# Performance work log

Hardware: AMD Instinct MI355X
Metric: run time of the kernel (lower is better)

## Reference

```python
import jax, jax.numpy as jnp
import numpy as np

GENRES = 20; TAGS = 1000; GTAGS = 1128; MOVIES = 20000; YEARS = 120; TBINS = 128
B = 1024; HIST = 50; PH = 256; OD = 128
EG = 8; ET = 16; EGT = 16; EM = 32; EY = 8; EUG = 32; ETS = 4
PAD = MOVIES  # padding index; context buffers have MOVIES+1 rows, last row = zeros


def setup_inputs():
    ks = iter(jax.random.split(jax.random.key(0), 64))
    nrm = lambda shp, s=0.1: (s * jax.random.normal(next(ks), shp)).astype(jnp.float32)
    P = MOVIES + 1
    genome_ctx = jax.random.uniform(next(ks), (P, GTAGS), dtype=jnp.float32).at[-1].set(0.0)
    genre_ctx = jax.random.uniform(next(ks), (P, GENRES), dtype=jnp.float32).at[-1].set(0.0)
    tag_ctx = jax.random.uniform(next(ks), (P, TAGS), dtype=jnp.float32).at[-1].set(0.0)
    year_ctx = jax.random.randint(next(ks), (P,), 0, YEARS).at[-1].set(0)
    return dict(
        user_genre_contexts=jax.random.uniform(next(ks), (B, GENRES), dtype=jnp.float32),
        user_watch_history=jax.random.randint(next(ks), (B, HIST), 0, P),
        user_watch_history_ratings=5.0 * jax.random.uniform(next(ks), (B, HIST), dtype=jnp.float32),
        timestamps=jax.random.randint(next(ks), (B,), 0, TBINS),
        target_movieId=jax.random.randint(next(ks), (B,), 0, MOVIES),
        genome_ctx=genome_ctx, genre_ctx=genre_ctx, tag_ctx=tag_ctx, year_ctx=year_ctx,
        item_emb=nrm((P, EM), 0.01).at[-1].set(0.0),  # padding_idx row zeroed
        year_emb_tab=nrm((YEARS, EY), 0.01),
        ts_emb_tab=nrm((TBINS, ETS), 0.01),
        w_item=nrm((EM, EM)), b_item=jnp.zeros((EM,), jnp.float32),
        w_genre=nrm((GENRES, EG)), b_genre=jnp.zeros((EG,), jnp.float32),
        w_tag=nrm((TAGS, ET)), b_tag=jnp.zeros((ET,), jnp.float32),
        w_genome=nrm((GTAGS, EGT)), b_genome=jnp.zeros((EGT,), jnp.float32),
        w_year=nrm((EY, EY)), b_year=jnp.zeros((EY,), jnp.float32),
        w_ugenre=nrm((GENRES, EUG)), b_ugenre=jnp.zeros((EUG,), jnp.float32),
        w_ts=nrm((ETS, ETS)), b_ts=jnp.zeros((ETS,), jnp.float32),
        w_up1=nrm((OD + EGT + EUG + ETS, PH)), b_up1=jnp.zeros((PH,), jnp.float32),
        w_up2=nrm((PH, OD)), b_up2=jnp.zeros((OD,), jnp.float32),
        w_ip1=nrm((EG + ET + EGT + EM + EY, PH)), b_ip1=jnp.zeros((PH,), jnp.float32),
        w_ip2=nrm((PH, OD)), b_ip2=jnp.zeros((OD,), jnp.float32),
    )


def reference(user_genre_contexts, user_watch_history, user_watch_history_ratings,
              timestamps, target_movieId, genome_ctx, genre_ctx, tag_ctx, year_ctx,
              item_emb, year_emb_tab, ts_emb_tab,
              w_item, b_item, w_genre, b_genre, w_tag, b_tag, w_genome, b_genome,
              w_year, b_year, w_ugenre, b_ugenre, w_ts, b_ts,
              w_up1, b_up1, w_up2, b_up2, w_ip1, b_ip1, w_ip2, b_ip2):
    lt = lambda x, W, b: jnp.tanh(x @ W + b)

    def item_tower(mg, mt, mgt, yr, ids):
        # concat of five small Linear+Tanh towers, then 2-layer projection MLP
        cat = jnp.concatenate([
            lt(mg, w_genre, b_genre), lt(mt, w_tag, b_tag), lt(mgt, w_genome, b_genome),
            lt(item_emb[ids], w_item, b_item), lt(year_emb_tab[yr], w_year, b_year)], axis=-1)
        return jax.nn.relu(cat @ w_ip1 + b_ip1) @ w_ip2 + b_ip2

    Bn, Hn = user_watch_history.shape
    pad_mask = (user_watch_history != PAD).astype(jnp.float32)[..., None]       # (B,H,1)
    rating_weights = user_watch_history_ratings[..., None] * pad_mask            # (B,H,1)
    weight_sum = jnp.clip(jnp.abs(rating_weights).sum(axis=1), 1e-6)             # (B,1)

    # item pool: full item-tower embeddings of watched movies, rating-weighted avg
    flat = user_watch_history.reshape(-1)
    embs = item_tower(genre_ctx[flat], tag_ctx[flat], genome_ctx[flat],
                      year_ctx[flat], flat).reshape(Bn, Hn, OD)
    item_pool = (embs * rating_weights).sum(axis=1) / weight_sum                 # (B,OD)

    # genome pool (kept separately in use_item_pool_for_history mode)
    genome_embs = lt(genome_ctx[user_watch_history], w_genome, b_genome)         # (B,H,EGT)
    genome_emb = (genome_embs * rating_weights).sum(axis=1) / weight_sum

    genre_emb = lt(user_genre_contexts, w_ugenre, b_ugenre)
    ts_emb = lt(ts_emb_tab[timestamps], w_ts, b_ts)
    user_cat = jnp.concatenate([item_pool, genome_emb, genre_emb, ts_emb], axis=1)
    user = jax.nn.relu(user_cat @ w_up1 + b_up1) @ w_up2 + b_up2                 # (B,OD)

    item = item_tower(genre_ctx[target_movieId], tag_ctx[target_movieId],
                      genome_ctx[target_movieId], year_ctx[target_movieId], target_movieId)
    return jnp.einsum('bd,bd->b', user, item)
```

## Files before the change

### kernel.cpp

```cpp
#include <hip/hip_runtime.h>
#include <hip/hip_bf16.h>

typedef __bf16 bf16x8 __attribute__((ext_vector_type(8)));
typedef __bf16 bf16x4 __attribute__((ext_vector_type(4)));
typedef float  f32x4  __attribute__((ext_vector_type(4)));

namespace {
constexpr int P       = 20001;
constexpr int NT_TILE = 1251;
constexpr int PROWS   = NT_TILE * 16;
constexpr int NGENRES = 20;
constexpr int NTAGS   = 1000;
constexpr int NGTAGS  = 1128;
constexpr int NB      = 1024;
constexpr int NH      = 50;
constexpr int PHID    = 256;
constexpr int OD      = 128;
constexpr int EG = 8, ET = 16, EGT = 16, EM = 32, EY = 8, EUG = 32, ETS = 4;
constexpr int PAD  = 20000;
constexpr int SC   = 104;
constexpr int SH   = 264;
constexpr int UC   = 192;
constexpr int UCS  = 200;
constexpr int KC_TAG  = 32;
constexpr int KC_GENF = 40;
constexpr int KC_IP1 = 3,  NT_IP1 = 16;
constexpr int KC_IP2 = 8,  NT_IP2 = 8;
constexpr int KC_UP1 = 6,  NT_UP1 = 16;
constexpr int KC_UP2 = 8,  NT_UP2 = 8;
}

static __device__ __forceinline__ f32x4 mfma16(bf16x8 a, bf16x8 b, f32x4 c) {
  return __builtin_amdgcn_mfma_f32_16x16x32_bf16(a, b, c, 0, 0, 0);
}

static __device__ __forceinline__ bf16x8 cvt8(float4 v0, float4 v1) {
  return (bf16x8){(__bf16)v0.x, (__bf16)v0.y, (__bf16)v0.z, (__bf16)v0.w,
                  (__bf16)v1.x, (__bf16)v1.y, (__bf16)v1.z, (__bf16)v1.w};
}

static __device__ __forceinline__ void gldlds(const void* g, void* l) {
  __builtin_amdgcn_global_load_lds(
      (const __attribute__((address_space(1))) void*)g,
      (__attribute__((address_space(3))) void*)l, 16, 0, 0);
}

__global__ __launch_bounds__(512) void setup_wf_kernel(
    const float* __restrict__ w_tag, const float* __restrict__ w_genome,
    const float* __restrict__ w_ip1, const float* __restrict__ w_ip2,
    const float* __restrict__ w_up1, const float* __restrict__ w_up2,
    __bf16* __restrict__ Wtf, __bf16* __restrict__ Wgf,
    __bf16* __restrict__ Wip1f, __bf16* __restrict__ Wip2f,
    __bf16* __restrict__ Wup1f, __bf16* __restrict__ Wup2f)
{
  const int b = blockIdx.x, t = threadIdx.x;
  const int l = t >> 3, j = t & 7;
  const int krow = (l >> 4) * 8 + j, l15 = l & 15;
  const float* src; __bf16* dst; int K, N, kc, nt;
  if (b < 32)        { src = w_tag;    dst = Wtf   + (long)b * 512;       K = NTAGS;  N = 16;  kc = b;      nt = 0; }
  else if (b < 72)   { int i = b - 32;  src = w_genome; dst = Wgf   + (long)i * 512; K = NGTAGS; N = 16;  kc = i;      nt = 0; }
  else if (b < 120)  { int i = b - 72;  src = w_ip1;    dst = Wip1f + (long)i * 512; K = 80;     N = 256; kc = i / 16; nt = i % 16; }
  else if (b < 184)  { int i = b - 120; src = w_ip2;    dst = Wip2f + (long)i * 512; K = 256;    N = 128; kc = i / 8;  nt = i % 8; }
  else if (b < 280)  { int i = b - 184; src = w_up1;    dst = Wup1f + (long)i * 512; K = 180;    N = 256; kc = i / 16; nt = i % 16; }
  else               { int i = b - 280; src = w_up2;    dst = Wup2f + (long)i * 512; K = 256;    N = 128; kc = i / 8;  nt = i % 8; }
  const int k = kc * 32 + krow, n = nt * 16 + l15;
  float v = (k < K) ? src[(long)k * N + n] : 0.f;
  dst[t] = (__bf16)v;
}

__global__ __launch_bounds__(256, 2) void tower_kernel(
    const float* __restrict__ tag_ctx, const float* __restrict__ genome_ctx,
    const float* __restrict__ genre_ctx, const int* __restrict__ year_ctx,
    const float* __restrict__ item_emb, const float* __restrict__ year_tab,
    const float* __restrict__ w_genre, const float* __restrict__ b_genre,
    const float* __restrict__ b_tag,   const float* __restrict__ b_genome,
    const float* __restrict__ w_item,  const float* __restrict__ b_item,
    const float* __restrict__ w_year,  const float* __restrict__ b_year,
    const float* __restrict__ b_ip1,   const float* __restrict__ b_ip2,
    const __bf16* __restrict__ Wtf,   const __bf16* __restrict__ Wgf,
    const __bf16* __restrict__ Wip1f, const __bf16* __restrict__ Wip2f,
    float* __restrict__ T, float* __restrict__ GT)
{
  __shared__ __align__(16) union {
    char tag[16 * 128 * 16];
    char gen[16 * 192 * 16];
  } u;
  __shared__ __align__(16) __bf16 s_cat[16][SC];
  __shared__ __align__(16) __bf16 s_h[16][SH];
  __shared__ __align__(16) f32x4  s_redT[3][64];
  __shared__ __align__(16) f32x4  s_redG[3][64];

  const int t = threadIdx.x, tile = blockIdx.x;
  const int wave = t >> 6, lane = t & 63, l15 = lane & 15, quad = lane >> 4;
  const int r = t >> 4, c16 = t & 15;
  const long rid_r = min(tile * 16 + r, P - 1);
  const int x = l15 & 7;

  f32x4 accT = {0.f, 0.f, 0.f, 0.f};
  f32x4 accG = {0.f, 0.f, 0.f, 0.f};

  #pragma unroll
  for (int h = 0; h < 2; ++h) {
    #pragma unroll
    for (int cc = 0; cc < 8; ++cc) {
      const int c = wave * 8 + cc, rr = c >> 1, i = c & 1;
      const long rid = min(tile * 16 + rr, P - 1);
      const char* rp = (const char*)tag_ctx + rid * (NTAGS * 4);
      const int gs = min(((i * 64 + lane) ^ (rr & 7)) + h * 128, 249);
      gldlds(rp + (long)gs * 16, u.tag + ((rr * 128 + i * 64) * 16));
    }
    asm volatile("s_waitcnt vmcnt(0)" ::: "memory");
    __syncthreads();
    #pragma unroll
    for (int c = 0; c < 4; ++c) {
      const int kcg = h * 16 + wave * 4 + c;
      const int j = (wave * 4 + c) * 8 + quad * 2;
      const float4* rowp = (const float4*)u.tag + l15 * 128;
      const float4 a0 = rowp[j ^ x];
      const float4 a1 = rowp[(j + 1) ^ x];
      bf16x8 tb = *(const bf16x8*)(Wtf + ((long)kcg * 64 + lane) * 8);
      accT = mfma16(cvt8(a0, a1), tb, accT);
    }
    __syncthreads();
  }

  #pragma unroll
  for (int h = 0; h < 2; ++h) {
    #pragma unroll
    for (int cc = 0; cc < 12; ++cc) {
      const int c = wave * 12 + cc, rr = c / 3, i = c % 3;
      const long rid = min(tile * 16 + rr, P - 1);
      const char* rp = (const char*)genome_ctx + rid * (NGTAGS * 4);
      const int gs = min(((i * 64 + lane) ^ (rr & 7)) + h * 160, 281);
      gldlds(rp + (long)gs * 16, u.gen + ((rr * 192 + i * 64) * 16));
    }
    asm volatile("s_waitcnt vmcnt(0)" ::: "memory");
    __syncthreads();
    #pragma unroll
    for (int c = 0; c < 5; ++c) {
      const int kcg = h * 20 + wave * 5 + c;
      const int j = (wave * 5 + c) * 8 + quad * 2;
      const float4* rowp = (const float4*)u.gen + l15 * 192;
      const float4 a0 = rowp[j ^ x];
      const float4 a1 = rowp[(j + 1) ^ x];
      bf16x8 gb = *(const bf16x8*)(Wgf + ((long)kcg * 64 + lane) * 8);
      accG = mfma16(cvt8(a0, a1), gb, accG);
    }
    __syncthreads();
  }

  if (wave > 0)  s_redT[wave - 1][lane] = accT;
  if (wave != 1) s_redG[wave ? wave - 1 : 0][lane] = accG;

  {
    const int m = r, j = c16;
    const long id = rid_r;
    if (j < 8) {
      const float* rg = genre_ctx + id * NGENRES;
      float a = b_genre[j];
      #pragma unroll
      for (int k = 0; k < NGENRES; ++k) a = fmaf(rg[k], w_genre[k * EG + j], a);
      s_cat[m][j] = (__bf16)tanhf(a);
      s_cat[m][80 + j] = (__bf16)0.f;
      s_cat[m][88 + j] = (__bf16)0.f;
    } else {
      const int jj = j - 8;
      const int yr = year_ctx[id];
      float a = b_year[jj];
      #pragma unroll
      for (int k = 0; k < EY; ++k)
        a = fmaf(year_tab[yr * EY + k], w_year[k * EY + jj], a);
      s_cat[m][72 + jj] = (__bf16)tanhf(a);
    }
    const float* e = item_emb + id * EM;
    float a0 = b_item[2 * j], a1 = b_item[2 * j + 1];
    #pragma unroll 8
    for (int k = 0; k < EM; ++k) {
      float ev = e[k];
      a0 = fmaf(ev, w_item[k * EM + 2 * j], a0);
      a1 = fmaf(ev, w_item[k * EM + 2 * j + 1], a1);
    }
    s_cat[m][40 + 2 * j]     = (__bf16)tanhf(a0);
    s_cat[m][40 + 2 * j + 1] = (__bf16)tanhf(a1);
  }
  __syncthreads();

  if (wave == 0) {
    accT += s_redT[0][lane]; accT += s_redT[1][lane]; accT += s_redT[2][lane];
    const float bt = b_tag[l15];
    #pragma unroll
    for (int r2 = 0; r2 < 4; ++r2)
      s_cat[quad * 4 + r2][EG + l15] = (__bf16)tanhf(accT[r2] + bt);
  } else if (wave == 1) {
    accG += s_redG[0][lane]; accG += s_redG[1][lane]; accG += s_redG[2][lane];
    const float bg = b_genome[l15];
    #pragma unroll
    for (int r2 = 0; r2 < 4; ++r2) {
      int m = quad * 4 + r2;
      float v = tanhf(accG[r2] + bg);
      s_cat[m][EG + ET + l15] = (__bf16)v;
      GT[(long)(tile * 16 + m) * EGT + l15] = v;
    }
  }
  __syncthreads();

  {
    bf16x8 af[KC_IP1];
    #pragma unroll
    for (int kc = 0; kc < KC_IP1; ++kc)
      af[kc] = *(const bf16x8*)&s_cat[l15][kc * 32 + quad * 8];
    #pragma unroll
    for (int nt = 0; nt < 4; ++nt) {
      const int n = wave * 64 + nt * 16 + l15;
      const float bb = b_ip1[n];
      f32x4 acc = {bb, bb, bb, bb};
      bf16x8 bfr[KC_IP1];
      #pragma unroll
      for (int kc = 0; kc < KC_IP1; ++kc)
        bfr[kc] = *(const bf16x8*)(Wip1f + ((long)(kc * NT_IP1 + wave * 4 + nt) * 64 + lane) * 8);
      #pragma unroll
      for (int kc = 0; kc < KC_IP1; ++kc)
        acc = mfma16(af[kc], bfr[kc], acc);
      #pragma unroll
      for (int r2 = 0; r2 < 4; ++r2)
        s_h[quad * 4 + r2][n] = (__bf16)fmaxf(acc[r2], 0.f);
    }
  }
  __syncthreads();

  {
    bf16x8 af[KC_IP2];
    #pragma unroll
    for (int kc = 0; kc < KC_IP2; ++kc)
      af[kc] = *(const bf16x8*)&s_h[l15][kc * 32 + quad * 8];
    #pragma unroll
    for (int nt = 0; nt < 2; ++nt) {
      const int n = wave * 32 + nt * 16 + l15;
      const float bb = b_ip2[n];
      f32x4 acc = {bb, bb, bb, bb};
      bf16x8 bfr[KC_IP2];
      #pragma unroll
      for (int kc = 0; kc < KC_IP2; ++kc)
        bfr[kc] = *(const bf16x8*)(Wip2f + ((long)(kc * NT_IP2 + wave * 2 + nt) * 64 + lane) * 8);
      #pragma unroll
      for (int kc = 0; kc < KC_IP2; ++kc)
        acc = mfma16(af[kc], bfr[kc], acc);
      #pragma unroll
      for (int r2 = 0; r2 < 4; ++r2)
        T[(long)(tile * 16 + quad * 4 + r2) * OD + n] = acc[r2];
    }
  }
}

__global__ __launch_bounds__(256) void user_pool_kernel(
    const float* __restrict__ ugc, const int* __restrict__ hist,
    const float* __restrict__ ratings, const int* __restrict__ tstamps,
    const float* __restrict__ ts_tab,
    const float* __restrict__ w_ugenre, const float* __restrict__ b_ugenre,
    const float* __restrict__ w_ts, const float* __restrict__ b_ts,
    const float* __restrict__ T, const float* __restrict__ GT,
    __bf16* __restrict__ Ucat)
{
  __shared__ float s_w[64];
  __shared__ int   s_ids[64];
  __shared__ float s_part[2][OD];
  __shared__ float s_gp[8][EGT];
  __shared__ float s_inv;

  const int b = blockIdx.x, t = threadIdx.x;

  if (t < 64) {
    int id = PAD; float w = 0.f;
    if (t < NH) {
      id = hist[b * NH + t];
      float r = ratings[b * NH + t];
      w = (id != PAD) ? r : 0.f;
    }
    s_ids[t] = id; s_w[t] = w;
    float s = fabsf(w);
    #pragma unroll
    for (int off = 32; off; off >>= 1) s += __shfl_xor(s, off, 64);
    if (t == 0) s_inv = 1.f / fmaxf(s, 1e-6f);
  }
  __syncthreads();
  const float inv = s_inv;

  {
    const int c = t & (OD - 1), part = t >> 7;
    float acc = 0.f;
    #pragma unroll
    for (int i = 0; i < 25; ++i) {
      const int h = part * 25 + i;
      acc = fmaf(s_w[h], T[(long)s_ids[h] * OD + c], acc);
    }
    s_part[part][c] = acc;
  }
  __syncthreads();
  if (t < OD) {
    Ucat[(long)b * UC + t] = (__bf16)((s_part[0][t] + s_part[1][t]) * inv);
  } else {
    const int uu = t - 128, col = uu & 15, part = uu >> 4;
    float acc = 0.f;
    #pragma unroll
    for (int i = 0; i < 7; ++i) {
      const int h = part * 7 + i;
      if (h < NH) acc = fmaf(s_w[h], GT[(long)s_ids[h] * EGT + col], acc);
    }
    s_gp[part][col] = acc;
  }
  __syncthreads();
  if (t < EGT) {
    float acc = 0.f;
    #pragma unroll
    for (int p = 0; p < 8; ++p) acc += s_gp[p][t];
    Ucat[(long)b * UC + OD + t] = (__bf16)(acc * inv);
  } else if (t >= 32 && t < 64) {
    const int j = t - 32;
    float a = b_ugenre[j];
    #pragma unroll
    for (int k = 0; k < NGENRES; ++k)
      a = fmaf(ugc[b * NGENRES + k], w_ugenre[k * EUG + j], a);
    Ucat[(long)b * UC + 144 + j] = (__bf16)tanhf(a);
  } else if (t >= 64 && t < 64 + ETS) {
    const int j = t - 64;
    const int ts = tstamps[b];
    float a = b_ts[j];
    #pragma unroll
    for (int k = 0; k < ETS; ++k)
      a = fmaf(ts_tab[ts * ETS + k], w_ts[k * ETS + j], a);
    Ucat[(long)b * UC + 176 + j] = (__bf16)tanhf(a);
  } else if (t >= 68 && t < 80) {
    Ucat[(long)b * UC + 180 + (t - 68)] = (__bf16)0.f;
  }
}

__global__ __launch_bounds__(256) void user_mlp_kernel(
    const int* __restrict__ target,
    const float* __restrict__ b_up1, const float* __restrict__ b_up2,
    const __bf16* __restrict__ Wup1f, const __bf16* __restrict__ Wup2f,
    const __bf16* __restrict__ Ucat, const float* __restrict__ T,
    float* __restrict__ out)
{
  __shared__ __align__(16) __bf16 s_u[16][UCS];
  __shared__ __align__(16) __bf16 s_h[16][SH];
  __shared__ __align__(16) float  s_e[16][132];

  const int t = threadIdx.x, blk = blockIdx.x;
  const int wave = t >> 6, lane = t & 63, l15 = lane & 15, quad = lane >> 4;
  const int u0 = blk * 16;

  {
    const int uu = t >> 4, s = t & 15;
    const __bf16* src = Ucat + (long)(u0 + uu) * UC;
    *(bf16x8*)&s_u[uu][s * 8] = *(const bf16x8*)(src + s * 8);
    if (s < 8)
      *(bf16x8*)&s_u[uu][(s + 16) * 8] = *(const bf16x8*)(src + (s + 16) * 8);
  }
  __syncthreads();

  {
    bf16x8 af[KC_UP1];
    #pragma unroll
    for (int kc = 0; kc < KC_UP1; ++kc)
      af[kc] = *(const bf16x8*)&s_u[l15][kc * 32 + quad * 8];
    #pragma unroll
    for (int nt = 0; nt < 4; ++nt) {
      const int n = wave * 64 + nt * 16 + l15;
      const float bb = b_up1[n];
      f32x4 acc = {bb, bb, bb, bb};
      bf16x8 bfr[KC_UP1];
      #pragma unroll
      for (int kc = 0; kc < KC_UP1; ++kc)
        bfr[kc] = *(const bf16x8*)(Wup1f + ((long)(kc * NT_UP1 + wave * 4 + nt) * 64 + lane) * 8);
      #pragma unroll
      for (int kc = 0; kc < KC_UP1; ++kc)
        acc = mfma16(af[kc], bfr[kc], acc);
      #pragma unroll
      for (int r2 = 0; r2 < 4; ++r2)
        s_h[quad * 4 + r2][n] = (__bf16)fmaxf(acc[r2], 0.f);
    }
  }
  __syncthreads();

  {
    bf16x8 af[KC_UP2];
    #pragma unroll
    for (int kc = 0; kc < KC_UP2; ++kc)
      af[kc] = *(const bf16x8*)&s_h[l15][kc * 32 + quad * 8];
    #pragma unroll
    for (int nt = 0; nt < 2; ++nt) {
      const int n = wave * 32 + nt * 16 + l15;
      const float bb = b_up2[n];
      f32x4 acc = {bb, bb, bb, bb};
      bf16x8 bfr[KC_UP2];
      #pragma unroll
      for (int kc = 0; kc < KC_UP2; ++kc)
        bfr[kc] = *(const bf16x8*)(Wup2f + ((long)(kc * NT_UP2 + wave * 2 + nt) * 64 + lane) * 8);
      #pragma unroll
      for (int kc = 0; kc < KC_UP2; ++kc)
        acc = mfma16(af[kc], bfr[kc], acc);
      #pragma unroll
      for (int r2 = 0; r2 < 4; ++r2)
        s_e[quad * 4 + r2][n] = acc[r2];
    }
  }
  __syncthreads();

  if (t < 128) {
    const int uu = t >> 3, q = t & 7;
    const int tgt = target[u0 + uu];
    const float* trow = T + (long)tgt * OD + q * 16;
    float s = 0.f;
    #pragma unroll
    for (int i = 0; i < 4; ++i) {
      float4 v = *(const float4*)(trow + i * 4);
      f32x4 e = *(const f32x4*)&s_e[uu][q * 16 + i * 4];
      s += v.x * e[0] + v.y * e[1] + v.z * e[2] + v.w * e[3];
    }
    s += __shfl_down(s, 1, 64);
    s += __shfl_down(s, 2, 64);
    s += __shfl_down(s, 4, 64);
    if (q == 0) out[u0 + uu] = s;
  }
}

extern "C" void kernel_launch(void* const* d_in, const int* in_sizes, int n_in,
                              void* d_out, int out_size, void* d_ws, size_t ws_size,
                              hipStream_t stream) {
  const float* ugc      = (const float*)d_in[0];
  const int*   hist     = (const int*)  d_in[1];
  const float* ratings  = (const float*)d_in[2];
  const int*   tstamps  = (const int*)  d_in[3];
  const int*   target   = (const int*)  d_in[4];
  const float* genome   = (const float*)d_in[5];
  const float* genrec   = (const float*)d_in[6];
  const float* tagc     = (const float*)d_in[7];
  const int*   yearc    = (const int*)  d_in[8];
  const float* item_emb = (const float*)d_in[9];
  const float* year_tab = (const float*)d_in[10];
  const float* ts_tab   = (const float*)d_in[11];
  const float* w_item   = (const float*)d_in[12];
  const float* b_item   = (const float*)d_in[13];
  const float* w_genre  = (const float*)d_in[14];
  const float* b_genre  = (const float*)d_in[15];
  const float* w_tag    = (const float*)d_in[16];
  const float* b_tag    = (const float*)d_in[17];
  const float* w_genome = (const float*)d_in[18];
  const float* b_genome = (const float*)d_in[19];
  const float* w_year   = (const float*)d_in[20];
  const float* b_year   = (const float*)d_in[21];
  const float* w_ugenre = (const float*)d_in[22];
  const float* b_ugenre = (const float*)d_in[23];
  const float* w_ts     = (const float*)d_in[24];
  const float* b_ts     = (const float*)d_in[25];
  const float* w_up1    = (const float*)d_in[26];
  const float* b_up1    = (const float*)d_in[27];
  const float* w_up2    = (const float*)d_in[28];
  const float* b_up2    = (const float*)d_in[29];
  const float* w_ip1    = (const float*)d_in[30];
  const float* b_ip1    = (const float*)d_in[31];
  const float* w_ip2    = (const float*)d_in[32];
  const float* b_ip2    = (const float*)d_in[33];

  char* ws = (char*)d_ws;
  size_t off = 0;
  float*  T     = (float*) (ws + off); off += (size_t)PROWS * OD * 4;
  float*  GT    = (float*) (ws + off); off += (size_t)PROWS * EGT * 4;
  __bf16* Ucat  = (__bf16*)(ws + off); off += (size_t)NB * UC * 2;
  __bf16* Wtf   = (__bf16*)(ws + off); off += (size_t)KC_TAG  * 512 * 2;
  __bf16* Wgf   = (__bf16*)(ws + off); off += (size_t)KC_GENF * 512 * 2;
  __bf16* Wip1f = (__bf16*)(ws + off); off += (size_t)KC_IP1 * NT_IP1 * 512 * 2;
  __bf16* Wip2f = (__bf16*)(ws + off); off += (size_t)KC_IP2 * NT_IP2 * 512 * 2;
  __bf16* Wup1f = (__bf16*)(ws + off); off += (size_t)KC_UP1 * NT_UP1 * 512 * 2;
  __bf16* Wup2f = (__bf16*)(ws + off); off += (size_t)KC_UP2 * NT_UP2 * 512 * 2;

  setup_wf_kernel<<<dim3(344), dim3(512), 0, stream>>>(
      w_tag, w_genome, w_ip1, w_ip2, w_up1, w_up2,
      Wtf, Wgf, Wip1f, Wip2f, Wup1f, Wup2f);

  tower_kernel<<<dim3(NT_TILE), dim3(256), 0, stream>>>(
      tagc, genome, genrec, yearc, item_emb, year_tab,
      w_genre, b_genre, b_tag, b_genome, w_item, b_item, w_year, b_year,
      b_ip1, b_ip2, Wtf, Wgf, Wip1f, Wip2f, T, GT);

  user_pool_kernel<<<dim3(NB), dim3(256), 0, stream>>>(
      ugc, hist, ratings, tstamps, ts_tab,
      w_ugenre, b_ugenre, w_ts, b_ts, T, GT, Ucat);

  user_mlp_kernel<<<dim3(NB / 16), dim3(256), 0, stream>>>(
      target, b_up1, b_up2, Wup1f, Wup2f, Ucat, T, (float*)d_out);
}
```

Baseline: 284.7 us.

## Fuse user pooling into user MLP kernel and drop Ucat buffer

Merges the per-user history pooling kernel into the user MLP kernel. Each 16-user block now gathers its own weighted item and genome embeddings and computes the genre and timestamp features directly into shared memory. This removes one kernel launch and the global round-trip through the bf16 Ucat buffer. The cost is that the gather now runs on 64 blocks instead of 1024, with each thread looping over 50 history rows, so the pooling phase has far less parallelism and may become latency bound.

```diff
diff --git a/kernel.cpp b/kernel.cpp
--- a/kernel.cpp
+++ b/kernel.cpp
@@ -20,7 +20,6 @@
 constexpr int PAD  = 20000;
 constexpr int SC   = 104;
 constexpr int SH   = 264;
-constexpr int UC   = 192;
 constexpr int UCS  = 200;
 constexpr int KC_TAG  = 32;
 constexpr int KC_GENF = 40;
@@ -252,109 +251,90 @@
   }
 }
 
-__global__ __launch_bounds__(256) void user_pool_kernel(
+__global__ __launch_bounds__(256) void user_kernel(
     const float* __restrict__ ugc, const int* __restrict__ hist,
     const float* __restrict__ ratings, const int* __restrict__ tstamps,
     const float* __restrict__ ts_tab,
     const float* __restrict__ w_ugenre, const float* __restrict__ b_ugenre,
     const float* __restrict__ w_ts, const float* __restrict__ b_ts,
-    const float* __restrict__ T, const float* __restrict__ GT,
-    __bf16* __restrict__ Ucat)
-{
-  __shared__ float s_w[64];
-  __shared__ int   s_ids[64];
-  __shared__ float s_part[2][OD];
-  __shared__ float s_gp[8][EGT];
-  __shared__ float s_inv;
-
-  const int b = blockIdx.x, t = threadIdx.x;
-
-  if (t < 64) {
-    int id = PAD; float w = 0.f;
-    if (t < NH) {
-      id = hist[b * NH + t];
-      float r = ratings[b * NH + t];
-      w = (id != PAD) ? r : 0.f;
-    }
-    s_ids[t] = id; s_w[t] = w;
-    float s = fabsf(w);
-    #pragma unroll
-    for (int off = 32; off; off >>= 1) s += __shfl_xor(s, off, 64);
-    if (t == 0) s_inv = 1.f / fmaxf(s, 1e-6f);
-  }
-  __syncthreads();
-  const float inv = s_inv;
-
-  {
-    const int c = t & (OD - 1), part = t >> 7;
-    float acc = 0.f;
-    #pragma unroll
-    for (int i = 0; i < 25; ++i) {
-      const int h = part * 25 + i;
-      acc = fmaf(s_w[h], T[(long)s_ids[h] * OD + c], acc);
-    }
-    s_part[part][c] = acc;
-  }
-  __syncthreads();
-  if (t < OD) {
-    Ucat[(long)b * UC + t] = (__bf16)((s_part[0][t] + s_part[1][t]) * inv);
-  } else {
-    const int uu = t - 128, col = uu & 15, part = uu >> 4;
-    float acc = 0.f;
-    #pragma unroll
-    for (int i = 0; i < 7; ++i) {
-      const int h = part * 7 + i;
-      if (h < NH) acc = fmaf(s_w[h], GT[(long)s_ids[h] * EGT + col], acc);
-    }
-    s_gp[part][col] = acc;
-  }
-  __syncthreads();
-  if (t < EGT) {
-    float acc = 0.f;
-    #pragma unroll
-    for (int p = 0; p < 8; ++p) acc += s_gp[p][t];
-    Ucat[(long)b * UC + OD + t] = (__bf16)(acc * inv);
-  } else if (t >= 32 && t < 64) {
-    const int j = t - 32;
-    float a = b_ugenre[j];
-    #pragma unroll
-    for (int k = 0; k < NGENRES; ++k)
-      a = fmaf(ugc[b * NGENRES + k], w_ugenre[k * EUG + j], a);
-    Ucat[(long)b * UC + 144 + j] = (__bf16)tanhf(a);
-  } else if (t >= 64 && t < 64 + ETS) {
-    const int j = t - 64;
-    const int ts = tstamps[b];
-    float a = b_ts[j];
-    #pragma unroll
-    for (int k = 0; k < ETS; ++k)
-      a = fmaf(ts_tab[ts * ETS + k], w_ts[k * ETS + j], a);
-    Ucat[(long)b * UC + 176 + j] = (__bf16)tanhf(a);
-  } else if (t >= 68 && t < 80) {
-    Ucat[(long)b * UC + 180 + (t - 68)] = (__bf16)0.f;
-  }
-}
-
-__global__ __launch_bounds__(256) void user_mlp_kernel(
     const int* __restrict__ target,
     const float* __restrict__ b_up1, const float* __restrict__ b_up2,
     const __bf16* __restrict__ Wup1f, const __bf16* __restrict__ Wup2f,
-    const __bf16* __restrict__ Ucat, const float* __restrict__ T,
+    const float* __restrict__ T, const float* __restrict__ GT,
     float* __restrict__ out)
 {
   __shared__ __align__(16) __bf16 s_u[16][UCS];
   __shared__ __align__(16) __bf16 s_h[16][SH];
   __shared__ __align__(16) float  s_e[16][132];
+  __shared__ float s_w[16][NH + 2];
+  __shared__ int   s_ids[16][NH + 2];
+  __shared__ float s_inv[16];
 
   const int t = threadIdx.x, blk = blockIdx.x;
   const int wave = t >> 6, lane = t & 63, l15 = lane & 15, quad = lane >> 4;
   const int u0 = blk * 16;
-
-  {
-    const int uu = t >> 4, s = t & 15;
-    const __bf16* src = Ucat + (long)(u0 + uu) * UC;
-    *(bf16x8*)&s_u[uu][s * 8] = *(const bf16x8*)(src + s * 8);
-    if (s < 8)
-      *(bf16x8*)&s_u[uu][(s + 16) * 8] = *(const bf16x8*)(src + (s + 16) * 8);
+  const int uu = t >> 4, q = t & 15;
+
+  {
+    float psum = 0.f;
+    for (int i = q; i < NH; i += 16) {
+      const int id = hist[(long)(u0 + uu) * NH + i];
+      const float rr = ratings[(long)(u0 + uu) * NH + i];
+      const float w = (id != PAD) ? rr : 0.f;
+      s_ids[uu][i] = id; s_w[uu][i] = w;
+      psum += fabsf(w);
+    }
+    psum += __shfl_xor(psum, 1, 64);
+    psum += __shfl_xor(psum, 2, 64);
+    psum += __shfl_xor(psum, 4, 64);
+    psum += __shfl_xor(psum, 8, 64);
+    if (q == 0) s_inv[uu] = 1.f / fmaxf(psum, 1e-6f);
+  }
+  __syncthreads();
+
+  {
+    const float inv = s_inv[uu];
+    const int c0 = q * 8;
+    float acc[8] = {0.f, 0.f, 0.f, 0.f, 0.f, 0.f, 0.f, 0.f};
+    float gacc = 0.f;
+    for (int h = 0; h < NH; ++h) {
+      const int id = s_ids[uu][h];
+      const float w = s_w[uu][h];
+      const float* trow = T + (long)id * OD + c0;
+      const float4 v0 = *(const float4*)trow;
+      const float4 v1 = *(const float4*)(trow + 4);
+      acc[0] = fmaf(w, v0.x, acc[0]); acc[1] = fmaf(w, v0.y, acc[1]);
+      acc[2] = fmaf(w, v0.z, acc[2]); acc[3] = fmaf(w, v0.w, acc[3]);
+      acc[4] = fmaf(w, v1.x, acc[4]); acc[5] = fmaf(w, v1.y, acc[5]);
+      acc[6] = fmaf(w, v1.z, acc[6]); acc[7] = fmaf(w, v1.w, acc[7]);
+      gacc = fmaf(w, GT[(long)id * EGT + q], gacc);
+    }
+    #pragma unroll
+    for (int j = 0; j < 8; ++j) s_u[uu][c0 + j] = (__bf16)(acc[j] * inv);
+    s_u[uu][OD + q] = (__bf16)(gacc * inv);
+  }
+
+  {
+    const float* ug = ugc + (long)(u0 + uu) * NGENRES;
+    #pragma unroll
+    for (int jj = 0; jj < 2; ++jj) {
+      const int j = q * 2 + jj;
+      float a = b_ugenre[j];
+      #pragma unroll
+      for (int k = 0; k < NGENRES; ++k)
+        a = fmaf(ug[k], w_ugenre[k * EUG + j], a);
+      s_u[uu][144 + j] = (__bf16)tanhf(a);
+    }
+  }
+  if (q < ETS) {
+    const int ts = tstamps[u0 + uu];
+    float a = b_ts[q];
+    #pragma unroll
+    for (int k = 0; k < ETS; ++k)
+      a = fmaf(ts_tab[ts * ETS + k], w_ts[k * ETS + q], a);
+    s_u[uu][176 + q] = (__bf16)tanhf(a);
+  } else {
+    s_u[uu][176 + q] = (__bf16)0.f;
   }
   __syncthreads();
 
@@ -407,20 +387,20 @@
   __syncthreads();
 
   if (t < 128) {
-    const int uu = t >> 3, q = t & 7;
-    const int tgt = target[u0 + uu];
-    const float* trow = T + (long)tgt * OD + q * 16;
+    const int us = t >> 3, q8 = t & 7;
+    const int tgt = target[u0 + us];
+    const float* trow = T + (long)tgt * OD + q8 * 16;
     float s = 0.f;
     #pragma unroll
     for (int i = 0; i < 4; ++i) {
       float4 v = *(const float4*)(trow + i * 4);
-      f32x4 e = *(const f32x4*)&s_e[uu][q * 16 + i * 4];
+      f32x4 e = *(const f32x4*)&s_e[us][q8 * 16 + i * 4];
       s += v.x * e[0] + v.y * e[1] + v.z * e[2] + v.w * e[3];
     }
     s += __shfl_down(s, 1, 64);
     s += __shfl_down(s, 2, 64);
     s += __shfl_down(s, 4, 64);
-    if (q == 0) out[u0 + uu] = s;
+    if (q8 == 0) out[u0 + us] = s;
   }
 }
 
@@ -466,7 +446,6 @@
   size_t off = 0;
   float*  T     = (float*) (ws + off); off += (size_t)PROWS * OD * 4;
   float*  GT    = (float*) (ws + off); off += (size_t)PROWS * EGT * 4;
-  __bf16* Ucat  = (__bf16*)(ws + off); off += (size_t)NB * UC * 2;
   __bf16* Wtf   = (__bf16*)(ws + off); off += (size_t)KC_TAG  * 512 * 2;
   __bf16* Wgf   = (__bf16*)(ws + off); off += (size_t)KC_GENF * 512 * 2;
   __bf16* Wip1f = (__bf16*)(ws + off); off += (size_t)KC_IP1 * NT_IP1 * 512 * 2;
@@ -483,10 +462,8 @@
       w_genre, b_genre, b_tag, b_genome, w_item, b_item, w_year, b_year,
       b_ip1, b_ip2, Wtf, Wgf, Wip1f, Wip2f, T, GT);
 
-  user_pool_kernel<<<dim3(NB), dim3(256), 0, stream>>>(
+  user_kernel<<<dim3(NB / 16), dim3(256), 0, stream>>>(
       ugc, hist, ratings, tstamps, ts_tab,
-      w_ugenre, b_ugenre, w_ts, b_ts, T, GT, Ucat);
-
-  user_mlp_kernel<<<dim3(NB / 16), dim3(256), 0, stream>>>(
-      target, b_up1, b_up2, Wup1f, Wup2f, Ucat, T, (float*)d_out);
-}
+      w_ugenre, b_ugenre, w_ts, b_ts,
+      target, b_up1, b_up2, Wup1f, Wup2f, T, GT, (float*)d_out);
+}
```

After: 283.4 us. About the same (-0.5%).
